# Kernel tuning notes

Measured on AMD Instinct MI355X. Metric: run time of the kernel, lower is better.

## Reference

```python
import jax, jax.numpy as jnp
import numpy as np

B, S, D, H, HD = 2, 2048, 768, 12, 64


def setup_inputs() -> dict:
    key = jax.random.key(0)
    ks = jax.random.split(key, 8)
    w = lambda k, shp: jax.random.normal(k, shp, dtype=jnp.float32) * 0.02
    return {
        "hidden_states": jax.random.normal(ks[0], (B, S, D), dtype=jnp.float32),
        "Wq": w(ks[1], (D, D)), "bq": jnp.zeros((D,), jnp.float32),
        "Wk": w(ks[2], (D, D)), "bk": jnp.zeros((D,), jnp.float32),
        "Wv": w(ks[3], (D, D)), "bv": jnp.zeros((D,), jnp.float32),
        # hedgehog feature maps are initialized to identity in the module
        "Wfq": jnp.eye(HD, dtype=jnp.float32) + w(ks[4], (HD, HD)),
        "bfq": jnp.zeros((HD,), jnp.float32),
        "Wfk": jnp.eye(HD, dtype=jnp.float32) + w(ks[5], (HD, HD)),
        "bfk": jnp.zeros((HD,), jnp.float32),
    }


def _heads(x):
    # [B,S,D] -> [B,H,S,HD]
    return x.reshape(B, S, H, HD).transpose(0, 2, 1, 3)


def _feature_map(x, Wf, bf):
    # exp / exp(-x) hedgehog map: [B,H,S,HD] -> [B,H,S,2*HD]
    y = jnp.einsum('bhsd,ed->bhse', x, Wf) + bf
    return jnp.concatenate([jnp.exp(y), jnp.exp(-y)], axis=-1)


def reference(hidden_states, Wq, bq, Wk, bk, Wv, bv, Wfq, bfq, Wfk, bfk):
    h = hidden_states
    q = _heads(h @ Wq.T + bq)   # [B,H,S,HD]
    k = _heads(h @ Wk.T + bk)
    v = _heads(h @ Wv.T + bv)

    # frozen base (softmax) attention producing outputs + true_attns
    scale = 1.0 / np.sqrt(HD).astype(np.float32)
    scores = jnp.einsum('bhmd,bhnd->bhmn', q, k) * scale
    true_attns = jax.nn.softmax(scores, axis=-1)
    out = jnp.einsum('bhmn,bhnd->bhmd', true_attns, v)
    outputs = out.transpose(0, 2, 1, 3).reshape(B, S, D)

    # hedgehog predicted attention: quadratic linear attention
    fq = _feature_map(q, Wfq, bfq)  # [B,H,S,2*HD]
    fk = _feature_map(k, Wfk, bfk)
    qk = jnp.einsum('bhmd,bhnd->bhmn', fq, fk)
    pred_attns = qk / qk.sum(axis=-1, keepdims=True)

    return outputs, pred_attns, true_attns
```

## Files before the change

### kernel.cpp

```cpp
#include <hip/hip_runtime.h>
#include <math.h>

namespace {

constexpr int kB = 2, kS = 2048, kD = 768, kH = 12, kHD = 64, kF = 128, kBH = kB * kH;

typedef __attribute__((ext_vector_type(8))) short short8;
typedef __attribute__((ext_vector_type(4))) short short4v;
typedef __attribute__((ext_vector_type(4))) float f32x4;

__device__ __forceinline__ ushort f2bf(float x) {
    union { float f; unsigned u; } v; v.f = x;
    return (ushort)((v.u + 0x7fffu + ((v.u >> 16) & 1u)) >> 16);
}
__device__ __forceinline__ float bf2f(ushort u) {
    union { unsigned u; float f; } v; v.u = ((unsigned)u) << 16; return v.f;
}

__device__ __forceinline__ void gload16(const ushort* g, void* lds) {
    __builtin_amdgcn_global_load_lds(
        (const __attribute__((address_space(1))) void*)g,
        (__attribute__((address_space(3))) void*)lds, 16, 0, 0);
}

__device__ __forceinline__ void gstage64x64(ushort* ldsBase, const ushort* g,
                                            size_t strideElems, int w, int lane) {
    #pragma unroll
    for (int j = 0; j < 2; ++j) {
        const int row = 16 * w + 8 * j + (lane >> 3);
        const int chunk = lane & 7;
        const ushort* gp = g + (size_t)row * strideElems + ((chunk ^ (row & 7)) * 8);
        void* lp = (char*)ldsBase + (16 * w + 8 * j) * 128;
        gload16(gp, lp);
    }
}

__device__ __forceinline__ void gstage64x128(ushort* ldsBase, const ushort* g,
                                             int w, int lane) {
    #pragma unroll
    for (int j = 0; j < 4; ++j) {
        const int row = 16 * w + 4 * j + (lane >> 4);
        const int chunk = lane & 15;
        const ushort* gp = g + (size_t)row * kF + ((chunk ^ (row & 7)) * 8);
        void* lp = (char*)ldsBase + (16 * w + 4 * j) * 256;
        gload16(gp, lp);
    }
}

__device__ __forceinline__ void stage64x64(ushort* dst, const ushort* srcRow0,
                                           size_t rowStride, int t) {
    const int row = t >> 2, ce = (t & 3) * 16;
    const ushort* s = srcRow0 + (size_t)row * rowStride + ce;
    uint4 u0 = *(const uint4*)s;
    uint4 u1 = *(const uint4*)(s + 8);
    const int sw = (row & 7) << 4;
    *(uint4*)((char*)dst + row * 128 + ((ce * 2) ^ sw)) = u0;
    *(uint4*)((char*)dst + row * 128 + ((ce * 2 + 16) ^ sw)) = u1;
}

__device__ __forceinline__ void stage64x128(ushort* dst, const ushort* srcRow0, int t) {
    const int row = t >> 2, ce = (t & 3) * 32;
    const ushort* s = srcRow0 + (size_t)row * kF + ce;
    const int sw = (row & 7) << 4;
    #pragma unroll
    for (int u = 0; u < 4; ++u) {
        uint4 x = *(const uint4*)(s + u * 8);
        *(uint4*)((char*)dst + row * 256 + ((ce * 2 + u * 16) ^ sw)) = x;
    }
}

__global__ __launch_bounds__(256) void cast_kernel(
    const float* __restrict__ s0, const float* __restrict__ s1,
    const float* __restrict__ s2, const float* __restrict__ s3,
    ushort* __restrict__ d0, ushort* __restrict__ d1,
    ushort* __restrict__ d2, ushort* __restrict__ d3)
{
    const int seg = blockIdx.y;
    const float* src = seg == 0 ? s0 : seg == 1 ? s1 : seg == 2 ? s2 : s3;
    ushort* dst      = seg == 0 ? d0 : seg == 1 ? d1 : seg == 2 ? d2 : d3;
    const int n4 = (seg == 0 ? kB * kS * kD : kD * kD) / 4;
    for (int i = blockIdx.x * 256 + threadIdx.x; i < n4; i += gridDim.x * 256) {
        float4 v = *(const float4*)&src[(size_t)i * 4];
        short4v o;
        o[0] = (short)f2bf(v.x); o[1] = (short)f2bf(v.y);
        o[2] = (short)f2bf(v.z); o[3] = (short)f2bf(v.w);
        *(short4v*)&dst[(size_t)i * 4] = o;
    }
}

__global__ __launch_bounds__(256) void qkv_mfma_kernel(
    const ushort* __restrict__ hb,
    const ushort* __restrict__ Wqb, const ushort* __restrict__ Wkb,
    const ushort* __restrict__ Wvb,
    const float* __restrict__ bq, const float* __restrict__ bk,
    const float* __restrict__ bv,
    const float* __restrict__ Wfq, const float* __restrict__ bfq,
    const float* __restrict__ Wfk, const float* __restrict__ bfk,
    ushort* __restrict__ qd, ushort* __restrict__ kd, ushort* __restrict__ vTd,
    ushort* __restrict__ fqd, ushort* __restrict__ fkd,
    float* __restrict__ part)
{
    const int which = blockIdx.z;
    const ushort* __restrict__ Wb  = which == 0 ? Wqb : which == 1 ? Wkb : Wvb;
    const float* __restrict__ bias = which == 0 ? bq : which == 1 ? bk : bv;

    const int m0 = blockIdx.x * 128;
    const int n0 = blockIdx.y * 64;
    const int t = threadIdx.x, lane = t & 63, w = t >> 6;
    const int g = lane >> 4, ln = lane & 15;

    __shared__ __align__(16) ushort As[128 * 64];
    __shared__ __align__(16) ushort Bs[64 * 64];
    __shared__ __align__(16) ushort Ws[64 * 64];
    __shared__ float zsum[4][128];

    if (which < 2) {
        const float* __restrict__ Wf = (which == 0) ? Wfq : Wfk;
        const int row = t >> 2, ce = (t & 3) * 16;
        ushort tmp[16];
        #pragma unroll
        for (int c = 0; c < 16; c += 4) {
            float4 u = *(const float4*)&Wf[(size_t)row * 64 + ce + c];
            tmp[c + 0] = f2bf(u.x); tmp[c + 1] = f2bf(u.y);
            tmp[c + 2] = f2bf(u.z); tmp[c + 3] = f2bf(u.w);
        }
        const int sw = (row & 7) << 4;
        *(uint4*)((char*)Ws + row * 128 + ((ce * 2) ^ sw)) = *(uint4*)&tmp[0];
        *(uint4*)((char*)Ws + row * 128 + ((ce * 2 + 16) ^ sw)) = *(uint4*)&tmp[8];
    }

    f32x4 acc[2][4];
    #pragma unroll
    for (int rs = 0; rs < 2; ++rs)
        #pragma unroll
        for (int nt = 0; nt < 4; ++nt) acc[rs][nt] = (f32x4){0.f, 0.f, 0.f, 0.f};

    for (int k0 = 0; k0 < kD; k0 += 64) {
        __syncthreads();
        #pragma unroll
        for (int u = 0; u < 4; ++u) {
            const int ci = u * 256 + t, row = ci >> 3, c = ci & 7;
            uint4 x = *(const uint4*)&hb[(size_t)(m0 + row) * kD + k0 + c * 8];
            *(uint4*)((char*)As + row * 128 + ((c * 16) ^ ((row & 7) << 4))) = x;
        }
        #pragma unroll
        for (int u = 0; u < 2; ++u) {
            const int ci = u * 256 + t, row = ci >> 3, c = ci & 7;
            uint4 x = *(const uint4*)&Wb[(size_t)(n0 + row) * kD + k0 + c * 8];
            *(uint4*)((char*)Bs + row * 128 + ((c * 16) ^ ((row & 7) << 4))) = x;
        }
        __syncthreads();

        short8 a[2][2], b[4][2];
        #pragma unroll
        for (int rs = 0; rs < 2; ++rs) {
            const int row = 32 * w + 16 * rs + ln, sw = (row & 7) << 4;
            #pragma unroll
            for (int kc = 0; kc < 2; ++kc)
                a[rs][kc] = *(const short8*)((const char*)As + row * 128 + ((kc * 64 + g * 16) ^ sw));
        }
        #pragma unroll
        for (int nt = 0; nt < 4; ++nt) {
            const int rk = nt * 16 + ln, sw = (rk & 7) << 4;
            #pragma unroll
            for (int kc = 0; kc < 2; ++kc)
                b[nt][kc] = *(const short8*)((const char*)Bs + rk * 128 + ((kc * 64 + g * 16) ^ sw));
        }
        #pragma unroll
        for (int rs = 0; rs < 2; ++rs)
            #pragma unroll
            for (int nt = 0; nt < 4; ++nt)
                #pragma unroll
                for (int kc = 0; kc < 2; ++kc)
                    acc[rs][nt] = __builtin_amdgcn_mfma_f32_16x16x32_bf16(
                        a[rs][kc], b[nt][kc], acc[rs][nt], 0, 0, 0);
    }

    const int hh = n0 >> 6;
    float bvn[4];
    #pragma unroll
    for (int nt = 0; nt < 4; ++nt) bvn[nt] = bias[n0 + nt * 16 + ln];

    if (which < 2) {
        ushort* __restrict__ dst = (which == 0) ? qd : kd;
        #pragma unroll
        for (int rs = 0; rs < 2; ++rs)
            #pragma unroll
            for (int nt = 0; nt < 4; ++nt)
                #pragma unroll
                for (int r = 0; r < 4; ++r) {
                    const int m = m0 + 32 * w + 16 * rs + g * 4 + r;
                    const int b_ = m >> 11, s_ = m & (kS - 1);
                    dst[((size_t)(b_ * kH + hh) * kS + s_) * kHD + nt * 16 + ln] =
                        f2bf(acc[rs][nt][r] + bvn[nt]);
                }
    } else {
        #pragma unroll
        for (int rs = 0; rs < 2; ++rs)
            #pragma unroll
            for (int nt = 0; nt < 4; ++nt) {
                const int m = m0 + 32 * w + 16 * rs + g * 4;
                const int b_ = m >> 11, s_ = m & (kS - 1);
                const int d = nt * 16 + ln;
                short4v o;
                #pragma unroll
                for (int r = 0; r < 4; ++r) o[r] = (short)f2bf(acc[rs][nt][r] + bvn[nt]);
                *(short4v*)&vTd[((size_t)(b_ * kH + hh) * kHD + d) * kS + s_] = o;
            }
    }

    if (which < 2) {
        __syncthreads();
        #pragma unroll
        for (int rs = 0; rs < 2; ++rs)
            #pragma unroll
            for (int nt = 0; nt < 4; ++nt)
                #pragma unroll
                for (int r = 0; r < 4; ++r) {
                    const int bm = 32 * w + 16 * rs + g * 4 + r;
                    const int e = nt * 16 + ln;
                    *(ushort*)((char*)As + bm * 128 + ((2 * e) ^ ((bm & 7) << 4))) =
                        f2bf(acc[rs][nt][r] + bvn[nt]);
                }
        __syncthreads();

        short8 a2[2][2], b2[4][2];
        #pragma unroll
        for (int rs = 0; rs < 2; ++rs) {
            const int row = 32 * w + 16 * rs + ln, sw = (row & 7) << 4;
            #pragma unroll
            for (int kc = 0; kc < 2; ++kc)
                a2[rs][kc] = *(const short8*)((const char*)As + row * 128 + ((kc * 64 + g * 16) ^ sw));
        }
        #pragma unroll
        for (int nt = 0; nt < 4; ++nt) {
            const int rk = nt * 16 + ln, sw = (rk & 7) << 4;
            #pragma unroll
            for (int kc = 0; kc < 2; ++kc)
                b2[nt][kc] = *(const short8*)((const char*)Ws + rk * 128 + ((kc * 64 + g * 16) ^ sw));
        }
        f32x4 yac[2][4];
        #pragma unroll
        for (int rs = 0; rs < 2; ++rs)
            #pragma unroll
            for (int nt = 0; nt < 4; ++nt) {
                yac[rs][nt] = (f32x4){0.f, 0.f, 0.f, 0.f};
                #pragma unroll
                for (int kc = 0; kc < 2; ++kc)
                    yac[rs][nt] = __builtin_amdgcn_mfma_f32_16x16x32_bf16(
                        a2[rs][kc], b2[nt][kc], yac[rs][nt], 0, 0, 0);
            }

        const float* __restrict__ bf2p = (which == 0) ? bfq : bfk;
        float bfv[4];
        #pragma unroll
        for (int nt = 0; nt < 4; ++nt) bfv[nt] = bf2p[nt * 16 + ln];

        ushort* __restrict__ dstF = (which == 0) ? fqd : fkd;
        float csp[4] = {0.f, 0.f, 0.f, 0.f}, csm[4] = {0.f, 0.f, 0.f, 0.f};
        #pragma unroll
        for (int rs = 0; rs < 2; ++rs)
            #pragma unroll
            for (int nt = 0; nt < 4; ++nt)
                #pragma unroll
                for (int r = 0; r < 4; ++r) {
                    const int m = m0 + 32 * w + 16 * rs + g * 4 + r;
                    const int b_ = m >> 11, s_ = m & (kS - 1);
                    const float y = yac[rs][nt][r] + bfv[nt];
                    const ushort hp = f2bf(__expf(y));
                    const ushort hm = f2bf(__expf(-y));
                    const size_t base =
                        ((size_t)(b_ * kH + hh) * kS + s_) * kF + nt * 16 + ln;
                    dstF[base] = hp;
                    dstF[base + 64] = hm;
                    if (which == 1) { csp[nt] += bf2f(hp); csm[nt] += bf2f(hm); }
                }

        if (which == 1) {
            #pragma unroll
            for (int nt = 0; nt < 4; ++nt) {
                csp[nt] += __shfl_xor(csp[nt], 16); csp[nt] += __shfl_xor(csp[nt], 32);
                csm[nt] += __shfl_xor(csm[nt], 16); csm[nt] += __shfl_xor(csm[nt], 32);
            }
            if (g == 0) {
                #pragma unroll
                for (int nt = 0; nt < 4; ++nt) {
                    zsum[w][nt * 16 + ln]      = csp[nt];
                    zsum[w][64 + nt * 16 + ln] = csm[nt];
                }
            }
            __syncthreads();
            if (t < 128) {
                const float s = zsum[0][t] + zsum[1][t] + zsum[2][t] + zsum[3][t];
                const int b_ = m0 >> 11, gr = (m0 & (kS - 1)) >> 7;
                part[((size_t)((b_ * kH + hh) * 16 + gr)) * kF + t] = s;
            }
        }
    }
}

__global__ __launch_bounds__(128) void fksum_red_kernel(
    const float* __restrict__ part, float* __restrict__ fksum)
{
    const int bh = blockIdx.x, e = threadIdx.x;
    float acc = 0.f;
    for (int g = 0; g < 16; ++g) acc += part[((size_t)bh * 16 + g) * kF + e];
    fksum[bh * kF + e] = acc;
}

__global__ __launch_bounds__(256) void true_attn_kernel(
    const ushort* __restrict__ q, const ushort* __restrict__ k,
    const ushort* __restrict__ vT,
    float* __restrict__ out0, float* __restrict__ out2)
{
    const int orig = blockIdx.y * 32 + blockIdx.x;
    const int swz  = (orig & 7) * 96 + (orig >> 3);
    const int bh = swz >> 5, m0 = (swz & 31) * 64;

    const int t = threadIdx.x, lane = t & 63, w = t >> 6;
    const int g = lane >> 4, ln = lane & 15;

    __shared__ __align__(16) ushort Qs[64 * 64];
    __shared__ __align__(16) ushort Ks[2][64 * 64];
    __shared__ __align__(16) ushort Vs[2][64 * 64];
    __shared__ __align__(16) ushort Ps[64 * 64];

    const ushort* __restrict__ qb = q  + (size_t)bh * kS * kHD;
    const ushort* __restrict__ kb = k  + (size_t)bh * kS * kHD;
    const ushort* __restrict__ vb = vT + (size_t)bh * kHD * kS;

    stage64x64(Qs, qb + (size_t)m0 * kHD, kHD, t);
    __syncthreads();

    short8 aq[2];
    {
        const int row = 16 * w + ln, sw = (row & 7) << 4;
        #pragma unroll
        for (int kc = 0; kc < 2; ++kc)
            aq[kc] = *(const short8*)((const char*)Qs + row * 128 + ((kc * 64 + g * 16) ^ sw));
    }

    gstage64x64(Ks[0], kb, kHD, w, lane);
    float zacc[4] = {0.f, 0.f, 0.f, 0.f};
    for (int tt = 0; tt < 32; ++tt) {
        const int cur = tt & 1;
        if (tt + 1 < 32) {
            gstage64x64(Ks[cur ^ 1], kb + (size_t)(tt + 1) * 64 * kHD, kHD, w, lane);
            asm volatile("s_waitcnt vmcnt(2)" ::: "memory");
        } else {
            asm volatile("s_waitcnt vmcnt(0)" ::: "memory");
        }
        __builtin_amdgcn_sched_barrier(0);
        __builtin_amdgcn_s_barrier();
        const ushort* KsC = Ks[cur];
        #pragma unroll
        for (int nt = 0; nt < 4; ++nt) {
            f32x4 c = {0.f, 0.f, 0.f, 0.f};
            const int rk = nt * 16 + ln, sw = (rk & 7) << 4;
            #pragma unroll
            for (int kc = 0; kc < 2; ++kc) {
                short8 b = *(const short8*)((const char*)KsC + rk * 128 + ((kc * 64 + g * 16) ^ sw));
                c = __builtin_amdgcn_mfma_f32_16x16x32_bf16(aq[kc], b, c, 0, 0, 0);
            }
            #pragma unroll
            for (int r = 0; r < 4; ++r) zacc[r] += __expf(c[r] * 0.125f);
        }
        __builtin_amdgcn_sched_barrier(0);
        __builtin_amdgcn_s_barrier();
    }
    float invl[4];
    #pragma unroll
    for (int r = 0; r < 4; ++r) {
        float z = zacc[r];
        z += __shfl_xor(z, 1); z += __shfl_xor(z, 2);
        z += __shfl_xor(z, 4); z += __shfl_xor(z, 8);
        invl[r] = 1.f / z;
    }

    f32x4 accv[4];
    #pragma unroll
    for (int dt = 0; dt < 4; ++dt) accv[dt] = (f32x4){0.f, 0.f, 0.f, 0.f};

    gstage64x64(Ks[0], kb, kHD, w, lane);
    gstage64x64(Vs[0], vb, kS, w, lane);
    for (int tt = 0; tt < 32; ++tt) {
        const int cur = tt & 1;
        const int n0 = tt * 64;
        if (tt + 1 < 32) {
            gstage64x64(Ks[cur ^ 1], kb + (size_t)(tt + 1) * 64 * kHD, kHD, w, lane);
            gstage64x64(Vs[cur ^ 1], vb + (tt + 1) * 64, kS, w, lane);
            asm volatile("s_waitcnt vmcnt(4)" ::: "memory");
        } else {
            asm volatile("s_waitcnt vmcnt(0)" ::: "memory");
        }
        __builtin_amdgcn_sched_barrier(0);
        __builtin_amdgcn_s_barrier();

        const ushort* KsC = Ks[cur];
        const ushort* VsC = Vs[cur];
        #pragma unroll
        for (int nt = 0; nt < 4; ++nt) {
            f32x4 c = {0.f, 0.f, 0.f, 0.f};
            const int rk = nt * 16 + ln, sw = (rk & 7) << 4;
            #pragma unroll
            for (int kc = 0; kc < 2; ++kc) {
                short8 b = *(const short8*)((const char*)KsC + rk * 128 + ((kc * 64 + g * 16) ^ sw));
                c = __builtin_amdgcn_mfma_f32_16x16x32_bf16(aq[kc], b, c, 0, 0, 0);
            }
            #pragma unroll
            for (int r = 0; r < 4; ++r) {
                const int prow = 16 * w + g * 4 + r;
                const float p = __expf(c[r] * 0.125f) * invl[r];
                out2[((size_t)bh * kS + m0 + prow) * kS + n0 + nt * 16 + ln] = p;
                const int pb = prow * 128 + ((2 * (nt * 16 + ln)) ^ ((prow & 7) << 4));
                *(ushort*)((char*)Ps + pb) = f2bf(p);
            }
        }
        asm volatile("s_waitcnt lgkmcnt(0)" ::: "memory");
        __builtin_amdgcn_sched_barrier(0);
        __builtin_amdgcn_s_barrier();

        const int rowp = 16 * w + ln, swp = (rowp & 7) << 4;
        #pragma unroll
        for (int kc = 0; kc < 2; ++kc) {
            short8 pa = *(const short8*)((const char*)Ps + rowp * 128 + ((kc * 64 + g * 16) ^ swp));
            #pragma unroll
            for (int dt = 0; dt < 4; ++dt) {
                const int rv = dt * 16 + ln, swv = (rv & 7) << 4;
                short8 bv = *(const short8*)((const char*)VsC + rv * 128 + ((kc * 64 + g * 16) ^ swv));
                accv[dt] = __builtin_amdgcn_mfma_f32_16x16x32_bf16(pa, bv, accv[dt], 0, 0, 0);
            }
        }
        __builtin_amdgcn_sched_barrier(0);
        __builtin_amdgcn_s_barrier();
    }

    const int b_ = bh / kH, h_ = bh % kH;
    #pragma unroll
    for (int dt = 0; dt < 4; ++dt)
        #pragma unroll
        for (int r = 0; r < 4; ++r) {
            const int prow = 16 * w + g * 4 + r;
            out0[((size_t)b_ * kS + m0 + prow) * kD + h_ * kHD + dt * 16 + ln] = accv[dt][r];
        }
}

__global__ __launch_bounds__(256) void pred_attn_kernel(
    const ushort* __restrict__ fq, const ushort* __restrict__ fk,
    const float* __restrict__ fksum, float* __restrict__ out1)
{
    const int orig = blockIdx.y * 32 + blockIdx.x;
    const int swz  = (orig & 7) * 96 + (orig >> 3);
    const int bh = swz >> 5, m0 = (swz & 31) * 64;

    const int t = threadIdx.x, lane = t & 63, w = t >> 6;
    const int g = lane >> 4, ln = lane & 15;

    __shared__ __align__(16) ushort Fq[64 * 128];
    __shared__ __align__(16) ushort Fk[2][64 * 128];
    __shared__ float fsum[128];
    __shared__ float invz[64];

    const ushort* __restrict__ fqb = fq + (size_t)bh * kS * kF;
    const ushort* __restrict__ fkb = fk + (size_t)bh * kS * kF;

    stage64x128(Fq, fqb + (size_t)m0 * kF, t);
    if (t < 128) fsum[t] = fksum[bh * kF + t];
    __syncthreads();

    short8 a[4];
    {
        const int row = 16 * w + ln, sw = (row & 7) << 4;
        #pragma unroll
        for (int kc = 0; kc < 4; ++kc)
            a[kc] = *(const short8*)((const char*)Fq + row * 256 + ((kc * 64 + g * 16) ^ sw));
    }

    float den = 0.f;
    #pragma unroll
    for (int kc = 0; kc < 4; ++kc)
        #pragma unroll
        for (int j = 0; j < 8; ++j)
            den += bf2f((ushort)a[kc][j]) * fsum[kc * 32 + g * 8 + j];
    den += __shfl_xor(den, 16);
    den += __shfl_xor(den, 32);
    if (g == 0) invz[16 * w + ln] = 1.f / den;
    __syncthreads();
    float invl[4];
    #pragma unroll
    for (int r = 0; r < 4; ++r) invl[r] = invz[16 * w + g * 4 + r];

    gstage64x128(Fk[0], fkb, w, lane);
    for (int tt = 0; tt < 32; ++tt) {
        const int cur = tt & 1;
        const int n0 = tt * 64;
        if (tt + 1 < 32) {
            gstage64x128(Fk[cur ^ 1], fkb + (size_t)(tt + 1) * 64 * kF, w, lane);
            asm volatile("s_waitcnt vmcnt(4)" ::: "memory");
        } else {
            asm volatile("s_waitcnt vmcnt(0)" ::: "memory");
        }
        __builtin_amdgcn_sched_barrier(0);
        __builtin_amdgcn_s_barrier();

        const ushort* FkC = Fk[cur];
        #pragma unroll
        for (int nt = 0; nt < 4; ++nt) {
            f32x4 c = {0.f, 0.f, 0.f, 0.f};
            const int rk = nt * 16 + ln, sw = (rk & 7) << 4;
            #pragma unroll
            for (int kc = 0; kc < 4; ++kc) {
                short8 b = *(const short8*)((const char*)FkC + rk * 256 + ((kc * 64 + g * 16) ^ sw));
                c = __builtin_amdgcn_mfma_f32_16x16x32_bf16(a[kc], b, c, 0, 0, 0);
            }
            #pragma unroll
            for (int r = 0; r < 4; ++r)
                out1[((size_t)bh * kS + m0 + 16 * w + g * 4 + r) * kS + n0 + nt * 16 + ln] =
                    c[r] * invl[r];
        }
        __builtin_amdgcn_sched_barrier(0);
        __builtin_amdgcn_s_barrier();
    }
}

}

extern "C" void kernel_launch(void* const* d_in, const int* in_sizes, int n_in,
                              void* d_out, int out_size, void* d_ws, size_t ws_size,
                              hipStream_t stream)
{
    (void)in_sizes; (void)n_in; (void)out_size; (void)ws_size;

    const float* hidden = (const float*)d_in[0];
    const float* Wq = (const float*)d_in[1];
    const float* bq = (const float*)d_in[2];
    const float* Wk = (const float*)d_in[3];
    const float* bk = (const float*)d_in[4];
    const float* Wv = (const float*)d_in[5];
    const float* bv = (const float*)d_in[6];
    const float* Wfq = (const float*)d_in[7];
    const float* bfq = (const float*)d_in[8];
    const float* Wfk = (const float*)d_in[9];
    const float* bfk = (const float*)d_in[10];

    float* out = (float*)d_out;
    float* out0 = out;
    float* out1 = out0 + (size_t)kB * kS * kD;
    float* out2 = out1 + (size_t)kBH * kS * kS;

    float* part = (float*)d_ws;
    float* fks  = part + (size_t)kBH * 16 * kF;
    ushort* hb  = (ushort*)(fks + (size_t)kBH * kF);
    ushort* Wqb = hb  + (size_t)kB * kS * kD;
    ushort* Wkb = Wqb + (size_t)kD * kD;
    ushort* Wvb = Wkb + (size_t)kD * kD;
    ushort* qw  = Wvb + (size_t)kD * kD;
    ushort* kw  = qw  + (size_t)kBH * kS * kHD;
    ushort* vTw = kw  + (size_t)kBH * kS * kHD;
    ushort* fqw = vTw + (size_t)kBH * kS * kHD;
    ushort* fkw = fqw + (size_t)kBH * kS * kF;

    cast_kernel<<<dim3(512, 4), 256, 0, stream>>>(
        hidden, Wq, Wk, Wv, hb, Wqb, Wkb, Wvb);
    qkv_mfma_kernel<<<dim3(kB * kS / 128, kD / 64, 3), 256, 0, stream>>>(
        hb, Wqb, Wkb, Wvb, bq, bk, bv,
        Wfq, bfq, Wfk, bfk,
        qw, kw, vTw, fqw, fkw, part);
    fksum_red_kernel<<<dim3(kBH), 128, 0, stream>>>(part, fks);
    true_attn_kernel<<<dim3(kS / 64, kBH), 256, 0, stream>>>(qw, kw, vTw, out0, out2);
    pred_attn_kernel<<<dim3(kS / 64, kBH), 256, 0, stream>>>(fqw, fkw, fks, out1);
}
```

Before: 314.2 us.

## Merge true and predicted attention kernels into one launch with role-split blocks

The softmax-attention and hedgehog-attention kernels become one kernel whose blocks take either role, chosen by a bit of the block index and interleaved in groups of eight. Both roles share a single 48KB LDS union buffer. The aim is to cut one launch and the tail gap between the two kernels, and to overlap the compute-heavy softmax blocks with the store-bound pred blocks on the same GPU. In exchange the pred role now reserves the larger LDS footprint (its own need was smaller), which may lower occupancy, and register allocation covers both branches.

```diff
diff --git a/kernel.cpp b/kernel.cpp
--- a/kernel.cpp
+++ b/kernel.cpp
@@ -308,218 +308,219 @@
     fksum[bh * kF + e] = acc;
 }
 
-__global__ __launch_bounds__(256) void true_attn_kernel(
+__global__ __launch_bounds__(256) void attn_fused_kernel(
     const ushort* __restrict__ q, const ushort* __restrict__ k,
     const ushort* __restrict__ vT,
-    float* __restrict__ out0, float* __restrict__ out2)
+    const ushort* __restrict__ fq, const ushort* __restrict__ fk,
+    const float* __restrict__ fksum,
+    float* __restrict__ out0, float* __restrict__ out1, float* __restrict__ out2)
 {
-    const int orig = blockIdx.y * 32 + blockIdx.x;
-    const int swz  = (orig & 7) * 96 + (orig >> 3);
+    const int orig = blockIdx.x;
+    const int which = (orig >> 3) & 1;
+    const int idx = (orig >> 4) * 8 + (orig & 7);
+    const int swz = (idx & 7) * 96 + (idx >> 3);
     const int bh = swz >> 5, m0 = (swz & 31) * 64;
 
     const int t = threadIdx.x, lane = t & 63, w = t >> 6;
     const int g = lane >> 4, ln = lane & 15;
 
-    __shared__ __align__(16) ushort Qs[64 * 64];
-    __shared__ __align__(16) ushort Ks[2][64 * 64];
-    __shared__ __align__(16) ushort Vs[2][64 * 64];
-    __shared__ __align__(16) ushort Ps[64 * 64];
-
-    const ushort* __restrict__ qb = q  + (size_t)bh * kS * kHD;
-    const ushort* __restrict__ kb = k  + (size_t)bh * kS * kHD;
-    const ushort* __restrict__ vb = vT + (size_t)bh * kHD * kS;
-
-    stage64x64(Qs, qb + (size_t)m0 * kHD, kHD, t);
-    __syncthreads();
-
-    short8 aq[2];
-    {
-        const int row = 16 * w + ln, sw = (row & 7) << 4;
-        #pragma unroll
-        for (int kc = 0; kc < 2; ++kc)
-            aq[kc] = *(const short8*)((const char*)Qs + row * 128 + ((kc * 64 + g * 16) ^ sw));
-    }
-
-    gstage64x64(Ks[0], kb, kHD, w, lane);
-    float zacc[4] = {0.f, 0.f, 0.f, 0.f};
-    for (int tt = 0; tt < 32; ++tt) {
-        const int cur = tt & 1;
-        if (tt + 1 < 32) {
-            gstage64x64(Ks[cur ^ 1], kb + (size_t)(tt + 1) * 64 * kHD, kHD, w, lane);
-            asm volatile("s_waitcnt vmcnt(2)" ::: "memory");
-        } else {
-            asm volatile("s_waitcnt vmcnt(0)" ::: "memory");
-        }
-        __builtin_amdgcn_sched_barrier(0);
-        __builtin_amdgcn_s_barrier();
-        const ushort* KsC = Ks[cur];
-        #pragma unroll
-        for (int nt = 0; nt < 4; ++nt) {
-            f32x4 c = {0.f, 0.f, 0.f, 0.f};
-            const int rk = nt * 16 + ln, sw = (rk & 7) << 4;
+    __shared__ __align__(16) ushort sbuf[24576];
+    __shared__ float smallf[192];
+
+    if (which == 0) {
+        ushort* Qs  = sbuf;
+        ushort* Ks0 = sbuf + 4096;
+        ushort* Ks1 = sbuf + 8192;
+        ushort* Vs0 = sbuf + 12288;
+        ushort* Vs1 = sbuf + 16384;
+        ushort* Ps  = sbuf + 20480;
+
+        const ushort* __restrict__ qb = q  + (size_t)bh * kS * kHD;
+        const ushort* __restrict__ kb = k  + (size_t)bh * kS * kHD;
+        const ushort* __restrict__ vb = vT + (size_t)bh * kHD * kS;
+
+        stage64x64(Qs, qb + (size_t)m0 * kHD, kHD, t);
+        __syncthreads();
+
+        short8 aq[2];
+        {
+            const int row = 16 * w + ln, sw = (row & 7) << 4;
+            #pragma unroll
+            for (int kc = 0; kc < 2; ++kc)
+                aq[kc] = *(const short8*)((const char*)Qs + row * 128 + ((kc * 64 + g * 16) ^ sw));
+        }
+
+        gstage64x64(Ks0, kb, kHD, w, lane);
+        float zacc[4] = {0.f, 0.f, 0.f, 0.f};
+        for (int tt = 0; tt < 32; ++tt) {
+            ushort* KsC = (tt & 1) ? Ks1 : Ks0;
+            ushort* KsN = (tt & 1) ? Ks0 : Ks1;
+            if (tt + 1 < 32) {
+                gstage64x64(KsN, kb + (size_t)(tt + 1) * 64 * kHD, kHD, w, lane);
+                asm volatile("s_waitcnt vmcnt(2)" ::: "memory");
+            } else {
+                asm volatile("s_waitcnt vmcnt(0)" ::: "memory");
+            }
+            __builtin_amdgcn_sched_barrier(0);
+            __builtin_amdgcn_s_barrier();
+            #pragma unroll
+            for (int nt = 0; nt < 4; ++nt) {
+                f32x4 c = {0.f, 0.f, 0.f, 0.f};
+                const int rk = nt * 16 + ln, sw = (rk & 7) << 4;
+                #pragma unroll
+                for (int kc = 0; kc < 2; ++kc) {
+                    short8 b = *(const short8*)((const char*)KsC + rk * 128 + ((kc * 64 + g * 16) ^ sw));
+                    c = __builtin_amdgcn_mfma_f32_16x16x32_bf16(aq[kc], b, c, 0, 0, 0);
+                }
+                #pragma unroll
+                for (int r = 0; r < 4; ++r) zacc[r] += __expf(c[r] * 0.125f);
+            }
+            __builtin_amdgcn_sched_barrier(0);
+            __builtin_amdgcn_s_barrier();
+        }
+        float invl[4];
+        #pragma unroll
+        for (int r = 0; r < 4; ++r) {
+            float z = zacc[r];
+            z += __shfl_xor(z, 1); z += __shfl_xor(z, 2);
+            z += __shfl_xor(z, 4); z += __shfl_xor(z, 8);
+            invl[r] = 1.f / z;
+        }
+
+        f32x4 accv[4];
+        #pragma unroll
+        for (int dt = 0; dt < 4; ++dt) accv[dt] = (f32x4){0.f, 0.f, 0.f, 0.f};
+
+        gstage64x64(Ks0, kb, kHD, w, lane);
+        gstage64x64(Vs0, vb, kS, w, lane);
+        for (int tt = 0; tt < 32; ++tt) {
+            const int n0 = tt * 64;
+            ushort* KsC = (tt & 1) ? Ks1 : Ks0;
+            ushort* VsC = (tt & 1) ? Vs1 : Vs0;
+            ushort* KsN = (tt & 1) ? Ks0 : Ks1;
+            ushort* VsN = (tt & 1) ? Vs0 : Vs1;
+            if (tt + 1 < 32) {
+                gstage64x64(KsN, kb + (size_t)(tt + 1) * 64 * kHD, kHD, w, lane);
+                gstage64x64(VsN, vb + (tt + 1) * 64, kS, w, lane);
+                asm volatile("s_waitcnt vmcnt(4)" ::: "memory");
+            } else {
+                asm volatile("s_waitcnt vmcnt(0)" ::: "memory");
+            }
+            __builtin_amdgcn_sched_barrier(0);
+            __builtin_amdgcn_s_barrier();
+
+            #pragma unroll
+            for (int nt = 0; nt < 4; ++nt) {
+                f32x4 c = {0.f, 0.f, 0.f, 0.f};
+                const int rk = nt * 16 + ln, sw = (rk & 7) << 4;
+                #pragma unroll
+                for (int kc = 0; kc < 2; ++kc) {
+                    short8 b = *(const short8*)((const char*)KsC + rk * 128 + ((kc * 64 + g * 16) ^ sw));
+                    c = __builtin_amdgcn_mfma_f32_16x16x32_bf16(aq[kc], b, c, 0, 0, 0);
+                }
+                #pragma unroll
+                for (int r = 0; r < 4; ++r) {
+                    const int prow = 16 * w + g * 4 + r;
+                    const float p = __expf(c[r] * 0.125f) * invl[r];
+                    out2[((size_t)bh * kS + m0 + prow) * kS + n0 + nt * 16 + ln] = p;
+                    const int pb = prow * 128 + ((2 * (nt * 16 + ln)) ^ ((prow & 7) << 4));
+                    *(ushort*)((char*)Ps + pb) = f2bf(p);
+                }
+            }
+            asm volatile("s_waitcnt lgkmcnt(0)" ::: "memory");
+            __builtin_amdgcn_sched_barrier(0);
+            __builtin_amdgcn_s_barrier();
+
+            const int rowp = 16 * w + ln, swp = (rowp & 7) << 4;
             #pragma unroll
             for (int kc = 0; kc < 2; ++kc) {
-                short8 b = *(const short8*)((const char*)KsC + rk * 128 + ((kc * 64 + g * 16) ^ sw));
-                c = __builtin_amdgcn_mfma_f32_16x16x32_bf16(aq[kc], b, c, 0, 0, 0);
-            }
-            #pragma unroll
-            for (int r = 0; r < 4; ++r) zacc[r] += __expf(c[r] * 0.125f);
-        }
-        __builtin_amdgcn_sched_barrier(0);
-        __builtin_amdgcn_s_barrier();
-    }
-    float invl[4];
-    #pragma unroll
-    for (int r = 0; r < 4; ++r) {
-        float z = zacc[r];
-        z += __shfl_xor(z, 1); z += __shfl_xor(z, 2);
-        z += __shfl_xor(z, 4); z += __shfl_xor(z, 8);
-        invl[r] = 1.f / z;
-    }
-
-    f32x4 accv[4];
-    #pragma unroll
-    for (int dt = 0; dt < 4; ++dt) accv[dt] = (f32x4){0.f, 0.f, 0.f, 0.f};
-
-    gstage64x64(Ks[0], kb, kHD, w, lane);
-    gstage64x64(Vs[0], vb, kS, w, lane);
-    for (int tt = 0; tt < 32; ++tt) {
-        const int cur = tt & 1;
-        const int n0 = tt * 64;
-        if (tt + 1 < 32) {
-            gstage64x64(Ks[cur ^ 1], kb + (size_t)(tt + 1) * 64 * kHD, kHD, w, lane);
-            gstage64x64(Vs[cur ^ 1], vb + (tt + 1) * 64, kS, w, lane);
-            asm volatile("s_waitcnt vmcnt(4)" ::: "memory");
-        } else {
-            asm volatile("s_waitcnt vmcnt(0)" ::: "memory");
-        }
-        __builtin_amdgcn_sched_barrier(0);
-        __builtin_amdgcn_s_barrier();
-
-        const ushort* KsC = Ks[cur];
-        const ushort* VsC = Vs[cur];
-        #pragma unroll
-        for (int nt = 0; nt < 4; ++nt) {
-            f32x4 c = {0.f, 0.f, 0.f, 0.f};
-            const int rk = nt * 16 + ln, sw = (rk & 7) << 4;
-            #pragma unroll
-            for (int kc = 0; kc < 2; ++kc) {
-                short8 b = *(const short8*)((const char*)KsC + rk * 128 + ((kc * 64 + g * 16) ^ sw));
-                c = __builtin_amdgcn_mfma_f32_16x16x32_bf16(aq[kc], b, c, 0, 0, 0);
-            }
+                short8 pa = *(const short8*)((const char*)Ps + rowp * 128 + ((kc * 64 + g * 16) ^ swp));
+                #pragma unroll
+                for (int dt = 0; dt < 4; ++dt) {
+                    const int rv = dt * 16 + ln, swv = (rv & 7) << 4;
+                    short8 bv = *(const short8*)((const char*)VsC + rv * 128 + ((kc * 64 + g * 16) ^ swv));
+                    accv[dt] = __builtin_amdgcn_mfma_f32_16x16x32_bf16(pa, bv, accv[dt], 0, 0, 0);
+                }
+            }
+            __builtin_amdgcn_sched_barrier(0);
+            __builtin_amdgcn_s_barrier();
+        }
+
+        const int b_ = bh / kH, h_ = bh % kH;
+        #pragma unroll
+        for (int dt = 0; dt < 4; ++dt)
             #pragma unroll
             for (int r = 0; r < 4; ++r) {
                 const int prow = 16 * w + g * 4 + r;
-                const float p = __expf(c[r] * 0.125f) * invl[r];
-                out2[((size_t)bh * kS + m0 + prow) * kS + n0 + nt * 16 + ln] = p;
-                const int pb = prow * 128 + ((2 * (nt * 16 + ln)) ^ ((prow & 7) << 4));
-                *(ushort*)((char*)Ps + pb) = f2bf(p);
-            }
-        }
-        asm volatile("s_waitcnt lgkmcnt(0)" ::: "memory");
-        __builtin_amdgcn_sched_barrier(0);
-        __builtin_amdgcn_s_barrier();
-
-        const int rowp = 16 * w + ln, swp = (rowp & 7) << 4;
-        #pragma unroll
-        for (int kc = 0; kc < 2; ++kc) {
-            short8 pa = *(const short8*)((const char*)Ps + rowp * 128 + ((kc * 64 + g * 16) ^ swp));
-            #pragma unroll
-            for (int dt = 0; dt < 4; ++dt) {
-                const int rv = dt * 16 + ln, swv = (rv & 7) << 4;
-                short8 bv = *(const short8*)((const char*)VsC + rv * 128 + ((kc * 64 + g * 16) ^ swv));
-                accv[dt] = __builtin_amdgcn_mfma_f32_16x16x32_bf16(pa, bv, accv[dt], 0, 0, 0);
-            }
-        }
-        __builtin_amdgcn_sched_barrier(0);
-        __builtin_amdgcn_s_barrier();
-    }
-
-    const int b_ = bh / kH, h_ = bh % kH;
-    #pragma unroll
-    for (int dt = 0; dt < 4; ++dt)
-        #pragma unroll
-        for (int r = 0; r < 4; ++r) {
-            const int prow = 16 * w + g * 4 + r;
-            out0[((size_t)b_ * kS + m0 + prow) * kD + h_ * kHD + dt * 16 + ln] = accv[dt][r];
-        }
-}
-
-__global__ __launch_bounds__(256) void pred_attn_kernel(
-    const ushort* __restrict__ fq, const ushort* __restrict__ fk,
-    const float* __restrict__ fksum, float* __restrict__ out1)
-{
-    const int orig = blockIdx.y * 32 + blockIdx.x;
-    const int swz  = (orig & 7) * 96 + (orig >> 3);
-    const int bh = swz >> 5, m0 = (swz & 31) * 64;
-
-    const int t = threadIdx.x, lane = t & 63, w = t >> 6;
-    const int g = lane >> 4, ln = lane & 15;
-
-    __shared__ __align__(16) ushort Fq[64 * 128];
-    __shared__ __align__(16) ushort Fk[2][64 * 128];
-    __shared__ float fsum[128];
-    __shared__ float invz[64];
-
-    const ushort* __restrict__ fqb = fq + (size_t)bh * kS * kF;
-    const ushort* __restrict__ fkb = fk + (size_t)bh * kS * kF;
-
-    stage64x128(Fq, fqb + (size_t)m0 * kF, t);
-    if (t < 128) fsum[t] = fksum[bh * kF + t];
-    __syncthreads();
-
-    short8 a[4];
-    {
-        const int row = 16 * w + ln, sw = (row & 7) << 4;
+                out0[((size_t)b_ * kS + m0 + prow) * kD + h_ * kHD + dt * 16 + ln] = accv[dt][r];
+            }
+    } else {
+        ushort* Fq  = sbuf;
+        ushort* Fk0 = sbuf + 8192;
+        ushort* Fk1 = sbuf + 16384;
+        float* fsum = smallf;
+        float* invz = smallf + 128;
+
+        const ushort* __restrict__ fqb = fq + (size_t)bh * kS * kF;
+        const ushort* __restrict__ fkb = fk + (size_t)bh * kS * kF;
+
+        stage64x128(Fq, fqb + (size_t)m0 * kF, t);
+        if (t < 128) fsum[t] = fksum[bh * kF + t];
+        __syncthreads();
+
+        short8 a[4];
+        {
+            const int row = 16 * w + ln, sw = (row & 7) << 4;
+            #pragma unroll
+            for (int kc = 0; kc < 4; ++kc)
+                a[kc] = *(const short8*)((const char*)Fq + row * 256 + ((kc * 64 + g * 16) ^ sw));
+        }
+
+        float den = 0.f;
         #pragma unroll
         for (int kc = 0; kc < 4; ++kc)
-            a[kc] = *(const short8*)((const char*)Fq + row * 256 + ((kc * 64 + g * 16) ^ sw));
-    }
-
-    float den = 0.f;
-    #pragma unroll
-    for (int kc = 0; kc < 4; ++kc)
-        #pragma unroll
-        for (int j = 0; j < 8; ++j)
-            den += bf2f((ushort)a[kc][j]) * fsum[kc * 32 + g * 8 + j];
-    den += __shfl_xor(den, 16);
-    den += __shfl_xor(den, 32);
-    if (g == 0) invz[16 * w + ln] = 1.f / den;
-    __syncthreads();
-    float invl[4];
-    #pragma unroll
-    for (int r = 0; r < 4; ++r) invl[r] = invz[16 * w + g * 4 + r];
-
-    gstage64x128(Fk[0], fkb, w, lane);
-    for (int tt = 0; tt < 32; ++tt) {
-        const int cur = tt & 1;
-        const int n0 = tt * 64;
-        if (tt + 1 < 32) {
-            gstage64x128(Fk[cur ^ 1], fkb + (size_t)(tt + 1) * 64 * kF, w, lane);
-            asm volatile("s_waitcnt vmcnt(4)" ::: "memory");
-        } else {
-            asm volatile("s_waitcnt vmcnt(0)" ::: "memory");
-        }
-        __builtin_amdgcn_sched_barrier(0);
-        __builtin_amdgcn_s_barrier();
-
-        const ushort* FkC = Fk[cur];
-        #pragma unroll
-        for (int nt = 0; nt < 4; ++nt) {
-            f32x4 c = {0.f, 0.f, 0.f, 0.f};
-            const int rk = nt * 16 + ln, sw = (rk & 7) << 4;
-            #pragma unroll
-            for (int kc = 0; kc < 4; ++kc) {
-                short8 b = *(const short8*)((const char*)FkC + rk * 256 + ((kc * 64 + g * 16) ^ sw));
-                c = __builtin_amdgcn_mfma_f32_16x16x32_bf16(a[kc], b, c, 0, 0, 0);
-            }
-            #pragma unroll
-            for (int r = 0; r < 4; ++r)
-                out1[((size_t)bh * kS + m0 + 16 * w + g * 4 + r) * kS + n0 + nt * 16 + ln] =
-                    c[r] * invl[r];
-        }
-        __builtin_amdgcn_sched_barrier(0);
-        __builtin_amdgcn_s_barrier();
+            #pragma unroll
+            for (int j = 0; j < 8; ++j)
+                den += bf2f((ushort)a[kc][j]) * fsum[kc * 32 + g * 8 + j];
+        den += __shfl_xor(den, 16);
+        den += __shfl_xor(den, 32);
+        if (g == 0) invz[16 * w + ln] = 1.f / den;
+        __syncthreads();
+        float invl[4];
+        #pragma unroll
+        for (int r = 0; r < 4; ++r) invl[r] = invz[16 * w + g * 4 + r];
+
+        gstage64x128(Fk0, fkb, w, lane);
+        for (int tt = 0; tt < 32; ++tt) {
+            const int n0 = tt * 64;
+            ushort* FkC = (tt & 1) ? Fk1 : Fk0;
+            ushort* FkN = (tt & 1) ? Fk0 : Fk1;
+            if (tt + 1 < 32) {
+                gstage64x128(FkN, fkb + (size_t)(tt + 1) * 64 * kF, w, lane);
+                asm volatile("s_waitcnt vmcnt(4)" ::: "memory");
+            } else {
+                asm volatile("s_waitcnt vmcnt(0)" ::: "memory");
+            }
+            __builtin_amdgcn_sched_barrier(0);
+            __builtin_amdgcn_s_barrier();
+
+            #pragma unroll
+            for (int nt = 0; nt < 4; ++nt) {
+                f32x4 c = {0.f, 0.f, 0.f, 0.f};
+                const int rk = nt * 16 + ln, sw = (rk & 7) << 4;
+                #pragma unroll
+                for (int kc = 0; kc < 4; ++kc) {
+                    short8 b = *(const short8*)((const char*)FkC + rk * 256 + ((kc * 64 + g * 16) ^ sw));
+                    c = __builtin_amdgcn_mfma_f32_16x16x32_bf16(a[kc], b, c, 0, 0, 0);
+                }
+                #pragma unroll
+                for (int r = 0; r < 4; ++r)
+                    out1[((size_t)bh * kS + m0 + 16 * w + g * 4 + r) * kS + n0 + nt * 16 + ln] =
+                        c[r] * invl[r];
+            }
+            __builtin_amdgcn_sched_barrier(0);
+            __builtin_amdgcn_s_barrier();
+        }
     }
 }
 
@@ -567,6 +568,6 @@
         Wfq, bfq, Wfk, bfk,
         qw, kw, vTw, fqw, fkw, part);
     fksum_red_kernel<<<dim3(kBH), 128, 0, stream>>>(part, fks);
-    true_attn_kernel<<<dim3(kS / 64, kBH), 256, 0, stream>>>(qw, kw, vTw, out0, out2);
-    pred_attn_kernel<<<dim3(kS / 64, kBH), 256, 0, stream>>>(fqw, fkw, fks, out1);
-}
+    attn_fused_kernel<<<dim3(2 * kS / 64 * kBH / 16 * 16), 256, 0, stream>>>(
+        qw, kw, vTw, fqw, fkw, fks, out0, out1, out2);
+}
```

Result: slower. 326.9 us (+4.1%).
